# Kernel optimization log

Measured on AMD Instinct MI355X. Metric: run time of the kernel, lower is better.

## Reference

```python
import jax, jax.numpy as jnp
import numpy as np
import math

B, C, H, W = 8, 256, 64, 64
G = 32           # norm_groups
IMG_C = 3        # image_channels * wavelet_components
EPS = 1e-5


def group_norm(x, gamma, beta):
    # x: [B, C, H, W]; normalize over (C//G, H, W) within each of G groups
    b, c, h, w = x.shape
    xg = x.reshape(b, G, c // G, h, w)
    mean = xg.mean(axis=(2, 3, 4), keepdims=True)
    var = xg.var(axis=(2, 3, 4), keepdims=True)
    xg = (xg - mean) * jax.lax.rsqrt(var + EPS)
    x = xg.reshape(b, c, h, w)
    return x * gamma[None, :, None, None] + beta[None, :, None, None]


def conv1x1(x, weight):
    # weight: [out_c, in_c]; 1x1 conv == channel matmul
    return jnp.einsum('oc,bchw->bohw', weight, x)


def setup_inputs() -> dict:
    key = jax.random.key(0)
    ks = jax.random.split(key, 8)
    s_q = 1.0 / math.sqrt(IMG_C)
    s_kv = 1.0 / math.sqrt(C)
    return {
        'input': jax.random.normal(ks[0], (B, C, H, W), jnp.float32),
        'quary': jax.random.normal(ks[1], (B, IMG_C, H, W), jnp.float32),
        'gn_weight': jnp.ones((C,), jnp.float32),
        'gn_bias': jnp.zeros((C,), jnp.float32),
        'w_q': jax.random.uniform(ks[2], (C, IMG_C), jnp.float32, -s_q, s_q),
        'w_kv': jax.random.uniform(ks[3], (2 * C, C), jnp.float32, -s_kv, s_kv),
        'w_out': jax.random.uniform(ks[4], (C, C), jnp.float32, -s_kv, s_kv),
        'b_out': jax.random.uniform(ks[5], (C,), jnp.float32, -s_kv, s_kv),
    }


def reference(input, quary, gn_weight, gn_bias, w_q, w_kv, w_out, b_out):
    b, c, h, w = input.shape
    norm = group_norm(input, gn_weight, gn_bias)
    kv = conv1x1(norm, w_kv)                      # [B, 2C, H, W]
    key_t, value = kv[:, :c], kv[:, c:]           # each [B, C, H, W]
    q = conv1x1(quary, w_q)                       # [B, C, H, W]
    # attention over all spatial positions, single head, head_dim = C
    attn = jnp.einsum('bchw,bcyx->bhwyx', q, key_t) / math.sqrt(c)
    attn = jax.nn.softmax(attn.reshape(b, h, w, h * w), axis=-1)
    attn = attn.reshape(b, h, w, h, w)
    out = jnp.einsum('bhwyx,bcyx->bchw', attn, value)  # [B, C, H, W]
    out = conv1x1(out, w_out) + b_out[None, :, None, None]
    return out + input
```

## Files before the change

### kernel.cpp

```cpp
#include <hip/hip_runtime.h>

typedef unsigned short u16;
typedef unsigned int   u32;
typedef float  f32x4  __attribute__((ext_vector_type(4)));
typedef float  fltx4  __attribute__((ext_vector_type(4)));
typedef float  f32x2  __attribute__((ext_vector_type(2)));
typedef short  bf16x8 __attribute__((ext_vector_type(8)));
typedef u32    u32x4  __attribute__((ext_vector_type(4)));
typedef u32    u32x2  __attribute__((ext_vector_type(2)));

#define CDIM 256
#define NPIX 4096
#define QSCALE 0.09016843736f

__device__ __forceinline__ u16 f2bf(float f) {
  u32 u = __builtin_bit_cast(u32, f);
  u += 0x7fffu + ((u >> 16) & 1u);
  return (u16)(u >> 16);
}
__device__ __forceinline__ float bf2f(u16 h) {
  return __builtin_bit_cast(float, (u32)h << 16);
}

#if __has_builtin(__builtin_amdgcn_exp2f)
#define FEXP2 __builtin_amdgcn_exp2f
#else
#define FEXP2 exp2f
#endif

#define LO2(v) __builtin_shufflevector(v, v, 0, 1)
#define HI2(v) __builtin_shufflevector(v, v, 2, 3)

union U8 { bf16x8 v; u16 u[8]; u32 w[4]; };

__device__ __forceinline__ void llds16(u16* lds_base, const u16* gsrc) {
  __builtin_amdgcn_global_load_lds(
      (const __attribute__((address_space(1))) unsigned int*)gsrc,
      (__attribute__((address_space(3))) unsigned int*)lds_base, 16, 0, 0);
}

__global__ __launch_bounds__(256) void prep(const float* __restrict__ wkv,
                                            const float* __restrict__ wout,
                                            const float* __restrict__ wq,
                                            u16* __restrict__ w16,
                                            float* __restrict__ wq3p) {
  const int blk = blockIdx.x, tid = threadIdx.x;
  if (blk < 4) {
    const float* s = (blk < 2 ? wkv + 65536 : wout) + (blk & 1) * 32768;
    u16* d = w16 + (blk >> 1) * 65536 + (blk & 1) * 32768;
    for (int i = tid * 4; i < 32768; i += 1024) {
      fltx4 v = *(const fltx4*)(s + i);
      u32x2 o;
      o[0] = (u32)f2bf(v[0]) | ((u32)f2bf(v[1]) << 16);
      o[1] = (u32)f2bf(v[2]) | ((u32)f2bf(v[3]) << 16);
      *(u32x2*)(d + i) = o;
    }
  } else {
    const int p = blk - 4, c = tid;
    float a0 = 0.f, a1 = 0.f, a2 = 0.f;
    for (int o = p * 64; o < p * 64 + 64; ++o) {
      float kv = wkv[o * 256 + c];
      a0 += wq[o * 3 + 0] * kv;
      a1 += wq[o * 3 + 1] * kv;
      a2 += wq[o * 3 + 2] * kv;
    }
    float* dst = wq3p + (p * 256 + c) * 4;
    dst[0] = a0 * QSCALE; dst[1] = a1 * QSCALE; dst[2] = a2 * QSCALE; dst[3] = 0.f;
  }
}

__global__ __launch_bounds__(1024) void gn_stats(const float* __restrict__ x,
                                                 float* __restrict__ stats) {
  int bg = blockIdx.x;
  const float* base = x + (long)bg * 32768;
  float s = 0.f, s2 = 0.f;
  for (int i = threadIdx.x; i < 8192; i += 1024) {
    fltx4 v = ((const fltx4*)base)[i];
    s  += v[0] + v[1] + v[2] + v[3];
    s2 += v[0]*v[0] + v[1]*v[1] + v[2]*v[2] + v[3]*v[3];
  }
  for (int off = 1; off < 64; off <<= 1) {
    s  += __shfl_xor(s, off);
    s2 += __shfl_xor(s2, off);
  }
  __shared__ float red[32];
  int w = threadIdx.x >> 6;
  if ((threadIdx.x & 63) == 0) { red[w] = s; red[16 + w] = s2; }
  __syncthreads();
  if (threadIdx.x < 16) {
    s  = red[threadIdx.x];
    s2 = red[16 + threadIdx.x];
    for (int off = 1; off < 16; off <<= 1) {
      s  += __shfl_xor(s, off);
      s2 += __shfl_xor(s2, off);
    }
    if (threadIdx.x == 0) {
      float mean = s * (1.f / 32768.f);
      float var  = s2 * (1.f / 32768.f) - mean * mean;
      stats[bg * 2]     = mean;
      stats[bg * 2 + 1] = rsqrtf(var + 1e-5f);
    }
  }
}

__global__ __launch_bounds__(256) void gn_apply(const float* __restrict__ x,
                                                const float* __restrict__ stats,
                                                const float* __restrict__ gamma,
                                                const float* __restrict__ beta,
                                                const float* __restrict__ wq3p,
                                                u16* __restrict__ normT,
                                                float* __restrict__ K3x,
                                                float* __restrict__ K3y,
                                                float* __restrict__ K3z) {
  __shared__ u16 tile[256 * 66];
  __shared__ float wl4[256 * 4];
  __shared__ float part[4][64][4];
  const int tid = threadIdx.x;
  const int b = blockIdx.y, nb = blockIdx.x * 64;
  const int nIn = tid & 63, c4 = tid >> 6;
  {
    const f32x4* wp = (const f32x4*)wq3p;
    *(f32x4*)&wl4[tid * 4] = wp[tid] + wp[256 + tid] + wp[512 + tid] + wp[768 + tid];
  }
  const float* xb = x + (long)b * (CDIM * NPIX);
  #pragma unroll 4
  for (int p = 0; p < 64; ++p) {
    int c = c4 * 64 + p;
    int g = c >> 3;
    float mean = stats[(b * 32 + g) * 2];
    float rstd = stats[(b * 32 + g) * 2 + 1];
    float v = xb[(long)c * NPIX + nb + nIn];
    tile[c * 66 + nIn] = f2bf((v - mean) * rstd * gamma[c] + beta[c]);
  }
  __syncthreads();
  u16* nT = normT + ((long)b * NPIX + nb) * CDIM;
  #pragma unroll 8
  for (int nl = 0; nl < 64; ++nl)
    nT[(long)nl * CDIM + tid] = tile[tid * 66 + nl];
  {
    float a0 = 0.f, a1 = 0.f, a2 = 0.f;
    #pragma unroll 8
    for (int cc = 0; cc < 64; ++cc) {
      int c = c4 * 64 + cc;
      float v = bf2f(tile[c * 66 + nIn]);
      const f32x4 wv = *(const f32x4*)&wl4[c * 4];
      a0 += v * wv[0]; a1 += v * wv[1]; a2 += v * wv[2];
    }
    part[c4][nIn][0] = a0; part[c4][nIn][1] = a1; part[c4][nIn][2] = a2;
  }
  __syncthreads();
  if (c4 == 0) {
    float s0 = part[0][nIn][0] + part[1][nIn][0] + part[2][nIn][0] + part[3][nIn][0];
    float s1 = part[0][nIn][1] + part[1][nIn][1] + part[2][nIn][1] + part[3][nIn][1];
    float s2 = part[0][nIn][2] + part[1][nIn][2] + part[2][nIn][2] + part[3][nIn][2];
    long idx = (long)b * NPIX + nb + nIn;
    K3x[idx] = s0; K3y[idx] = s1; K3z[idx] = s2;
  }
}

template <bool FINAL, bool MERGE>
__global__ __launch_bounds__(256, 2) void gemm_nt(
    const void* __restrict__ Ap, const void* __restrict__ Bp,
    const void* __restrict__ Bp2, const float* __restrict__ ls,
    void* __restrict__ Dp,
    const float* __restrict__ bias, const float* __restrict__ resid,
    int M, int N, long aBS, long bBS, long dBS, long rBS) {
  __shared__ u16 Als[128 * 72];
  __shared__ u16 Bls[128 * 72];
  __shared__ float invB[128];
  const int tid = threadIdx.x;
  const int lane = tid & 63;
  const int m = lane & 15, quad = lane >> 4;
  const int wid = tid >> 6;
  const int wm = wid & 1, wn = wid >> 1;
  const int m0 = blockIdx.x * 128, n0 = blockIdx.y * 128;
  const int bz = blockIdx.z;

  if constexpr (MERGE) {
    if (tid < 128) {
      long n = (long)bz * 4096 + n0 + tid;
      invB[tid] = 1.f / (ls[n] + ls[32768 + n]);
    }
    __syncthreads();
  }

  f32x4 acc[4][4] = {};

  for (int ks = 0; ks < 4; ++ks) {
    const int kb = ks * 64;
    if (ks) __syncthreads();
    {
      const u16* src = (const u16*)Ap + aBS * bz;
      #pragma unroll
      for (int it = 0; it < 4; ++it) {
        int idx = it * 2048 + tid * 8;
        int r = idx >> 6, c = idx & 63;
        *(u32x4*)&Als[r * 72 + c] = *(const u32x4*)(src + (long)(m0 + r) * CDIM + kb + c);
      }
    }
    if constexpr (MERGE) {
      const u16* s0 = (const u16*)Bp  + bBS * bz;
      const u16* s1 = (const u16*)Bp2 + bBS * bz;
      #pragma unroll
      for (int it = 0; it < 4; ++it) {
        int idx = it * 2048 + tid * 8;
        int r = idx >> 6, c = idx & 63;
        long off = (long)(n0 + r) * CDIM + kb + c;
        u32x4 A  = *(const u32x4*)(s0 + off);
        u32x4 Bq = *(const u32x4*)(s1 + off);
        float inv = invB[r];
        u32x4 o;
        #pragma unroll
        for (int i = 0; i < 4; ++i) {
          float lo = (bf2f((u16)(A[i] & 0xffff)) + bf2f((u16)(Bq[i] & 0xffff))) * inv;
          float hi = (bf2f((u16)(A[i] >> 16))    + bf2f((u16)(Bq[i] >> 16)))    * inv;
          o[i] = (u32)f2bf(lo) | ((u32)f2bf(hi) << 16);
        }
        *(u32x4*)&Bls[r * 72 + c] = o;
      }
    } else {
      const u16* src = (const u16*)Bp + bBS * bz;
      #pragma unroll
      for (int it = 0; it < 4; ++it) {
        int idx = it * 2048 + tid * 8;
        int r = idx >> 6, c = idx & 63;
        *(u32x4*)&Bls[r * 72 + c] = *(const u32x4*)(src + (long)(n0 + r) * CDIM + kb + c);
      }
    }
    __syncthreads();
    #pragma unroll
    for (int s = 0; s < 2; ++s) {
      bf16x8 av[4], bv[4];
      #pragma unroll
      for (int i = 0; i < 4; ++i)
        av[i] = *(const bf16x8*)&Als[(wm * 64 + i * 16 + m) * 72 + s * 32 + quad * 8];
      #pragma unroll
      for (int i = 0; i < 4; ++i)
        bv[i] = *(const bf16x8*)&Bls[(wn * 64 + i * 16 + m) * 72 + s * 32 + quad * 8];
      #pragma unroll
      for (int mi = 0; mi < 4; ++mi)
        #pragma unroll
        for (int ni = 0; ni < 4; ++ni)
          acc[mi][ni] = __builtin_amdgcn_mfma_f32_16x16x32_bf16(av[mi], bv[ni], acc[mi][ni], 0, 0, 0);
    }
  }

  const int row0 = m0 + wm * 64;
  const int col0 = n0 + wn * 64 + m;
  if constexpr (FINAL) {
    float* out = (float*)Dp + dBS * bz;
    const float* res = resid + rBS * bz;
    #pragma unroll
    for (int mi = 0; mi < 4; ++mi)
      #pragma unroll
      for (int r = 0; r < 4; ++r) {
        int row = row0 + mi * 16 + quad * 4 + r;
        float bs = bias[row];
        #pragma unroll
        for (int ni = 0; ni < 4; ++ni) {
          long off = (long)row * N + col0 + ni * 16;
          out[off] = acc[mi][ni][r] + bs + res[off];
        }
      }
  } else {
    u16* out = (u16*)Dp + dBS * bz;
    #pragma unroll
    for (int mi = 0; mi < 4; ++mi)
      #pragma unroll
      for (int r = 0; r < 4; ++r) {
        int row = row0 + mi * 16 + quad * 4 + r;
        #pragma unroll
        for (int ni = 0; ni < 4; ++ni)
          out[(long)row * N + col0 + ni * 16] = f2bf(acc[mi][ni][r]);
      }
  }
}

#define MFMA16(a, bfr, c) __builtin_amdgcn_mfma_f32_16x16x32_bf16(a, bfr, c, 0, 0, 0)

#define P_LOAD(ks, JB)                                                      \
  {                                                                         \
    const int jo_ = (JB) + (ks) * 32 + quad * 8;                            \
    kx0 = *(const fltx4*)(Kx + jo_); kx1 = *(const fltx4*)(Kx + jo_ + 4);   \
    ky0 = *(const fltx4*)(Ky + jo_); ky1 = *(const fltx4*)(Ky + jo_ + 4);   \
    kz0 = *(const fltx4*)(Kz + jo_); kz1 = *(const fltx4*)(Kz + jo_ + 4);   \
  }

#define P_EXP(PB, ks)                                                       \
  {                                                                         \
    f32x2 xc_[4] = {LO2(kx0), HI2(kx0), LO2(kx1), HI2(kx1)};                \
    f32x2 yc_[4] = {LO2(ky0), HI2(ky0), LO2(ky1), HI2(ky1)};                \
    f32x2 zc_[4] = {LO2(kz0), HI2(kz0), LO2(kz1), HI2(kz1)};                \
    _Pragma("unroll")                                                       \
    for (int qm_ = 0; qm_ < 2; ++qm_) {                                     \
      _Pragma("unroll")                                                     \
      for (int c2_ = 0; c2_ < 4; ++c2_) {                                   \
        f32x2 s_ = xc_[c2_] * y2[qm_][0] + yc_[c2_] * y2[qm_][1]            \
                 + zc_[c2_] * y2[qm_][2];                                   \
        float p0_ = FEXP2(s_[0]);                                           \
        float p1_ = FEXP2(s_[1]);                                           \
        u32 r0_ = __builtin_bit_cast(u32, p0_) + 0x8000u;                   \
        u32 r1_ = __builtin_bit_cast(u32, p1_) + 0x8000u;                   \
        PB[qm_][ks].w[c2_] = (r0_ >> 16) | (r1_ & 0xffff0000u);             \
        f32x2 pv_; pv_[0] = p0_; pv_[1] = p1_;                              \
        lsv[qm_] += pv_;                                                    \
      }                                                                     \
    }                                                                       \
  }

#define PV_GROUP(PB, CT0)                                                   \
  _Pragma("unroll")                                                         \
  for (int ct_ = (CT0); ct_ < (CT0) + 4; ++ct_) {                           \
    int c_ = ct_ * 16 + m;                                                  \
    bf16x8 a0_ = *(const bf16x8*)&Vb[c_ * 64 + (((quad)     ^ (c_ & 7)) << 3)]; \
    bf16x8 a1_ = *(const bf16x8*)&Vb[c_ * 64 + (((4 + quad) ^ (c_ & 7)) << 3)]; \
    acc[0][ct_] = MFMA16(a0_, PB[0][0].v, acc[0][ct_]);                     \
    acc[1][ct_] = MFMA16(a0_, PB[1][0].v, acc[1][ct_]);                     \
    acc[0][ct_] = MFMA16(a1_, PB[0][1].v, acc[0][ct_]);                     \
    acc[1][ct_] = MFMA16(a1_, PB[1][1].v, acc[1][ct_]);                     \
  }

__global__ __launch_bounds__(256, 2) void attn_kernel(
    const float* __restrict__ quary,
    const float* __restrict__ K3x, const float* __restrict__ K3y,
    const float* __restrict__ K3z,
    const u16* __restrict__ V, u16* __restrict__ Op0, u16* __restrict__ Op1,
    float* __restrict__ lsum) {
  __shared__ u16 VLS[2][256 * 64];
  const int lane = threadIdx.x & 63, w = threadIdx.x >> 6;
  const int m = lane & 15, quad = lane >> 4;
  const int b = blockIdx.z, half = blockIdx.y;
  const int qb = blockIdx.x * 128 + w * 32;

  f32x2 y2[2][3];
  #pragma unroll
  for (int qm = 0; qm < 2; ++qm) {
    int n = qb + qm * 16 + m;
    float q0 = quary[b * 12288 + n];
    float q1 = quary[b * 12288 + 4096 + n];
    float q2 = quary[b * 12288 + 8192 + n];
    y2[qm][0][0] = q0; y2[qm][0][1] = q0;
    y2[qm][1][0] = q1; y2[qm][1][1] = q1;
    y2[qm][2][0] = q2; y2[qm][2][1] = q2;
  }

  const float* Kx = K3x + (long)b * NPIX + half * 2048;
  const float* Ky = K3y + (long)b * NPIX + half * 2048;
  const float* Kz = K3z + (long)b * NPIX + half * 2048;
  const u16* VG = V + (long)b * CDIM * NPIX + half * 2048;

  int srcV[8];
  #pragma unroll
  for (int i = 0; i < 8; ++i) {
    int c = (w * 8 + i) * 8 + (lane >> 3);
    srcV[i] = c * NPIX + (((lane & 7) ^ (c & 7)) << 3);
  }

  f32x2 lsv[2] = {};
  f32x4 acc[2][16] = {};
  U8 pbA[2][2], pbB[2][2];
  fltx4 kx0, kx1, ky0, ky1, kz0, kz1;

  #pragma unroll
  for (int i = 0; i < 8; ++i)
    llds16(VLS[0] + (w * 8 + i) * 512, VG + srcV[i]);

  P_LOAD(0, 0); P_EXP(pbA, 0);
  P_LOAD(1, 0); P_EXP(pbA, 1);

  for (int kt = 0; kt < 31; ++kt) {
    __syncthreads();
    #pragma unroll
    for (int i = 0; i < 8; ++i)
      llds16(VLS[(kt + 1) & 1] + (w * 8 + i) * 512, VG + srcV[i] + (kt + 1) * 64);
    const u16* Vb = VLS[kt & 1];
    const int JB = (kt + 1) * 64;

    P_LOAD(0, JB);
    PV_GROUP(pbA, 0);
    PV_GROUP(pbA, 4);
    P_EXP(pbB, 0);
    P_LOAD(1, JB);
    PV_GROUP(pbA, 8);
    PV_GROUP(pbA, 12);
    P_EXP(pbB, 1);

    pbA[0][0] = pbB[0][0]; pbA[0][1] = pbB[0][1];
    pbA[1][0] = pbB[1][0]; pbA[1][1] = pbB[1][1];
  }
  {
    __syncthreads();
    const u16* Vb = VLS[1];
    PV_GROUP(pbA, 0);
    PV_GROUP(pbA, 4);
    PV_GROUP(pbA, 8);
    PV_GROUP(pbA, 12);
  }

  u16* OpB = (half ? Op1 : Op0);
  #pragma unroll
  for (int qm = 0; qm < 2; ++qm) {
    int n = qb + qm * 16 + m;
    u16* row = OpB + ((long)b * NPIX + n) * CDIM + quad * 4;
    #pragma unroll
    for (int ct = 0; ct < 16; ++ct) {
      u32x2 o;
      o[0] = (u32)f2bf(acc[qm][ct][0]) | ((u32)f2bf(acc[qm][ct][1]) << 16);
      o[1] = (u32)f2bf(acc[qm][ct][2]) | ((u32)f2bf(acc[qm][ct][3]) << 16);
      *(u32x2*)(row + ct * 16) = o;
    }
    float ls = lsv[qm][0] + lsv[qm][1];
    ls += __shfl_xor(ls, 16);
    ls += __shfl_xor(ls, 32);
    if (lane < 16)
      lsum[(long)half * 32768 + (long)b * NPIX + n] = ls;
  }
}

extern "C" void kernel_launch(void* const* d_in, const int* in_sizes, int n_in,
                              void* d_out, int out_size, void* d_ws, size_t ws_size,
                              hipStream_t stream) {
  (void)in_sizes; (void)n_in; (void)out_size; (void)ws_size;
  const float* input = (const float*)d_in[0];
  const float* quary = (const float*)d_in[1];
  const float* gnw   = (const float*)d_in[2];
  const float* gnb   = (const float*)d_in[3];
  const float* wq    = (const float*)d_in[4];
  const float* wkv   = (const float*)d_in[5];
  const float* wout  = (const float*)d_in[6];
  const float* bout  = (const float*)d_in[7];
  float* out = (float*)d_out;

  char* ws = (char*)d_ws;
  float* stats = (float*)ws;
  float* wq3p  = (float*)(ws + 4096);
  float* lsum  = (float*)(ws + 20480);
  float* K3x   = (float*)(ws + 282624);
  float* K3y   = (float*)(ws + 413696);
  float* K3z   = (float*)(ws + 544768);
  u16* w16   = (u16*)(ws + 675840);
  u16* normT = (u16*)(ws + 937984);
  u16* Vv    = (u16*)(ws + 937984 + 1L * 16777216);
  u16* Op0   = normT;
  u16* Op1   = (u16*)(ws + 937984 + 2L * 16777216);

  const long S = (long)NPIX * CDIM;

  prep<<<8, 256, 0, stream>>>(wkv, wout, wq, w16, wq3p);
  gn_stats<<<256, 1024, 0, stream>>>(input, stats);
  gn_apply<<<dim3(64, 8), 256, 0, stream>>>(input, stats, gnw, gnb, wq3p,
                                            normT, K3x, K3y, K3z);
  gemm_nt<false, false><<<dim3(2, 32, 8), 256, 0, stream>>>(
      w16, normT, nullptr, nullptr, Vv, nullptr, nullptr, 256, 4096, 0, S, S, 0);
  attn_kernel<<<dim3(32, 2, 8), 256, 0, stream>>>(quary, K3x, K3y, K3z, Vv, Op0, Op1, lsum);
  gemm_nt<true, true><<<dim3(2, 32, 8), 256, 0, stream>>>(
      w16 + 65536, Op0, Op1, lsum, out, bout, input, 256, 4096, 0, S, S, S);
}
```

Before: 240.5 us.

## Split attention work across 8 waves with 16 query rows each

The attention kernel now launches 512 threads per block, and each of the 8 waves handles 16 query rows instead of 32. This halves the per-thread accumulator and P-fragment register footprint, which allows higher occupancy (launch bounds 512,4). The exp computation is split into finer half-steps interleaved with the PV MFMA groups. In exchange, each V tile loaded into LDS is reused by each wave across fewer queries per MFMA operand load, which doubles the LDS read traffic per unit of compute.

```diff
diff --git a/kernel.cpp b/kernel.cpp
--- a/kernel.cpp
+++ b/kernel.cpp
@@ -278,49 +278,47 @@
 
 #define MFMA16(a, bfr, c) __builtin_amdgcn_mfma_f32_16x16x32_bf16(a, bfr, c, 0, 0, 0)
 
-#define P_LOAD(ks, JB)                                                      \
+#define PH_LOAD(ks, h)                                                      \
   {                                                                         \
-    const int jo_ = (JB) + (ks) * 32 + quad * 8;                            \
-    kx0 = *(const fltx4*)(Kx + jo_); kx1 = *(const fltx4*)(Kx + jo_ + 4);   \
-    ky0 = *(const fltx4*)(Ky + jo_); ky1 = *(const fltx4*)(Ky + jo_ + 4);   \
-    kz0 = *(const fltx4*)(Kz + jo_); kz1 = *(const fltx4*)(Kz + jo_ + 4);   \
-  }
-
-#define P_EXP(PB, ks)                                                       \
+    const int jo_ = JB + (ks) * 32 + quad * 8 + (h) * 4;                    \
+    kxa = *(const fltx4*)(Kx + jo_);                                        \
+    kya = *(const fltx4*)(Ky + jo_);                                        \
+    kza = *(const fltx4*)(Kz + jo_);                                        \
+  }
+
+#define PH_EXP(PB, ks, h)                                                   \
   {                                                                         \
-    f32x2 xc_[4] = {LO2(kx0), HI2(kx0), LO2(kx1), HI2(kx1)};                \
-    f32x2 yc_[4] = {LO2(ky0), HI2(ky0), LO2(ky1), HI2(ky1)};                \
-    f32x2 zc_[4] = {LO2(kz0), HI2(kz0), LO2(kz1), HI2(kz1)};                \
-    _Pragma("unroll")                                                       \
-    for (int qm_ = 0; qm_ < 2; ++qm_) {                                     \
-      _Pragma("unroll")                                                     \
-      for (int c2_ = 0; c2_ < 4; ++c2_) {                                   \
-        f32x2 s_ = xc_[c2_] * y2[qm_][0] + yc_[c2_] * y2[qm_][1]            \
-                 + zc_[c2_] * y2[qm_][2];                                   \
-        float p0_ = FEXP2(s_[0]);                                           \
-        float p1_ = FEXP2(s_[1]);                                           \
-        u32 r0_ = __builtin_bit_cast(u32, p0_) + 0x8000u;                   \
-        u32 r1_ = __builtin_bit_cast(u32, p1_) + 0x8000u;                   \
-        PB[qm_][ks].w[c2_] = (r0_ >> 16) | (r1_ & 0xffff0000u);             \
-        f32x2 pv_; pv_[0] = p0_; pv_[1] = p1_;                              \
-        lsv[qm_] += pv_;                                                    \
-      }                                                                     \
-    }                                                                       \
-  }
-
-#define PV_GROUP(PB, CT0)                                                   \
+    f32x2 xc0_ = LO2(kxa), xc1_ = HI2(kxa);                                 \
+    f32x2 yc0_ = LO2(kya), yc1_ = HI2(kya);                                 \
+    f32x2 zc0_ = LO2(kza), zc1_ = HI2(kza);                                 \
+    f32x2 s0_ = xc0_ * y2[0] + yc0_ * y2[1] + zc0_ * y2[2];                 \
+    f32x2 s1_ = xc1_ * y2[0] + yc1_ * y2[1] + zc1_ * y2[2];                 \
+    float p0_ = FEXP2(s0_[0]);                                              \
+    float p1_ = FEXP2(s0_[1]);                                              \
+    float p2_ = FEXP2(s1_[0]);                                              \
+    float p3_ = FEXP2(s1_[1]);                                              \
+    u32 r0_ = __builtin_bit_cast(u32, p0_) + 0x8000u;                       \
+    u32 r1_ = __builtin_bit_cast(u32, p1_) + 0x8000u;                       \
+    u32 r2_ = __builtin_bit_cast(u32, p2_) + 0x8000u;                       \
+    u32 r3_ = __builtin_bit_cast(u32, p3_) + 0x8000u;                       \
+    PB[ks].w[(h) * 2]     = (r0_ >> 16) | (r1_ & 0xffff0000u);              \
+    PB[ks].w[(h) * 2 + 1] = (r2_ >> 16) | (r3_ & 0xffff0000u);              \
+    f32x2 pa_; pa_[0] = p0_; pa_[1] = p1_;                                  \
+    f32x2 pb_; pb_[0] = p2_; pb_[1] = p3_;                                  \
+    lsv += pa_ + pb_;                                                       \
+  }
+
+#define PV_G(PB, CT0)                                                       \
   _Pragma("unroll")                                                         \
   for (int ct_ = (CT0); ct_ < (CT0) + 4; ++ct_) {                           \
     int c_ = ct_ * 16 + m;                                                  \
     bf16x8 a0_ = *(const bf16x8*)&Vb[c_ * 64 + (((quad)     ^ (c_ & 7)) << 3)]; \
     bf16x8 a1_ = *(const bf16x8*)&Vb[c_ * 64 + (((4 + quad) ^ (c_ & 7)) << 3)]; \
-    acc[0][ct_] = MFMA16(a0_, PB[0][0].v, acc[0][ct_]);                     \
-    acc[1][ct_] = MFMA16(a0_, PB[1][0].v, acc[1][ct_]);                     \
-    acc[0][ct_] = MFMA16(a1_, PB[0][1].v, acc[0][ct_]);                     \
-    acc[1][ct_] = MFMA16(a1_, PB[1][1].v, acc[1][ct_]);                     \
-  }
-
-__global__ __launch_bounds__(256, 2) void attn_kernel(
+    acc[ct_] = MFMA16(a0_, PB[0].v, acc[ct_]);                              \
+    acc[ct_] = MFMA16(a1_, PB[1].v, acc[ct_]);                              \
+  }
+
+__global__ __launch_bounds__(512, 4) void attn_kernel(
     const float* __restrict__ quary,
     const float* __restrict__ K3x, const float* __restrict__ K3y,
     const float* __restrict__ K3z,
@@ -330,18 +328,17 @@
   const int lane = threadIdx.x & 63, w = threadIdx.x >> 6;
   const int m = lane & 15, quad = lane >> 4;
   const int b = blockIdx.z, half = blockIdx.y;
-  const int qb = blockIdx.x * 128 + w * 32;
-
-  f32x2 y2[2][3];
-  #pragma unroll
-  for (int qm = 0; qm < 2; ++qm) {
-    int n = qb + qm * 16 + m;
+  const int qb = blockIdx.x * 128 + w * 16;
+
+  f32x2 y2[3];
+  {
+    int n = qb + m;
     float q0 = quary[b * 12288 + n];
     float q1 = quary[b * 12288 + 4096 + n];
     float q2 = quary[b * 12288 + 8192 + n];
-    y2[qm][0][0] = q0; y2[qm][0][1] = q0;
-    y2[qm][1][0] = q1; y2[qm][1][1] = q1;
-    y2[qm][2][0] = q2; y2[qm][2][1] = q2;
+    y2[0][0] = q0; y2[0][1] = q0;
+    y2[1][0] = q1; y2[1][1] = q1;
+    y2[2][0] = q2; y2[2][1] = q2;
   }
 
   const float* Kx = K3x + (long)b * NPIX + half * 2048;
@@ -349,67 +346,74 @@
   const float* Kz = K3z + (long)b * NPIX + half * 2048;
   const u16* VG = V + (long)b * CDIM * NPIX + half * 2048;
 
-  int srcV[8];
+  int srcV[4];
   #pragma unroll
-  for (int i = 0; i < 8; ++i) {
-    int c = (w * 8 + i) * 8 + (lane >> 3);
+  for (int i = 0; i < 4; ++i) {
+    int c = (w * 4 + i) * 8 + (lane >> 3);
     srcV[i] = c * NPIX + (((lane & 7) ^ (c & 7)) << 3);
   }
 
-  f32x2 lsv[2] = {};
-  f32x4 acc[2][16] = {};
-  U8 pbA[2][2], pbB[2][2];
-  fltx4 kx0, kx1, ky0, ky1, kz0, kz1;
+  f32x2 lsv = {};
+  f32x4 acc[16] = {};
+  U8 pbA[2], pbB[2];
+  fltx4 kxa, kya, kza;
 
   #pragma unroll
-  for (int i = 0; i < 8; ++i)
-    llds16(VLS[0] + (w * 8 + i) * 512, VG + srcV[i]);
-
-  P_LOAD(0, 0); P_EXP(pbA, 0);
-  P_LOAD(1, 0); P_EXP(pbA, 1);
+  for (int i = 0; i < 4; ++i)
+    llds16(VLS[0] + (w * 4 + i) * 512, VG + srcV[i]);
+
+  {
+    const int JB = 0;
+    PH_LOAD(0, 0); PH_EXP(pbA, 0, 0);
+    PH_LOAD(0, 1); PH_EXP(pbA, 0, 1);
+    PH_LOAD(1, 0); PH_EXP(pbA, 1, 0);
+    PH_LOAD(1, 1); PH_EXP(pbA, 1, 1);
+  }
 
   for (int kt = 0; kt < 31; ++kt) {
     __syncthreads();
     #pragma unroll
-    for (int i = 0; i < 8; ++i)
-      llds16(VLS[(kt + 1) & 1] + (w * 8 + i) * 512, VG + srcV[i] + (kt + 1) * 64);
+    for (int i = 0; i < 4; ++i)
+      llds16(VLS[(kt + 1) & 1] + (w * 4 + i) * 512, VG + srcV[i] + (kt + 1) * 64);
     const u16* Vb = VLS[kt & 1];
     const int JB = (kt + 1) * 64;
 
-    P_LOAD(0, JB);
-    PV_GROUP(pbA, 0);
-    PV_GROUP(pbA, 4);
-    P_EXP(pbB, 0);
-    P_LOAD(1, JB);
-    PV_GROUP(pbA, 8);
-    PV_GROUP(pbA, 12);
-    P_EXP(pbB, 1);
-
-    pbA[0][0] = pbB[0][0]; pbA[0][1] = pbB[0][1];
-    pbA[1][0] = pbB[1][0]; pbA[1][1] = pbB[1][1];
+    PH_LOAD(0, 0);
+    PV_G(pbA, 0);
+    PH_EXP(pbB, 0, 0);
+    PH_LOAD(0, 1);
+    PV_G(pbA, 4);
+    PH_EXP(pbB, 0, 1);
+    PH_LOAD(1, 0);
+    PV_G(pbA, 8);
+    PH_EXP(pbB, 1, 0);
+    PH_LOAD(1, 1);
+    PV_G(pbA, 12);
+    PH_EXP(pbB, 1, 1);
+
+    pbA[0] = pbB[0]; pbA[1] = pbB[1];
   }
   {
     __syncthreads();
     const u16* Vb = VLS[1];
-    PV_GROUP(pbA, 0);
-    PV_GROUP(pbA, 4);
-    PV_GROUP(pbA, 8);
-    PV_GROUP(pbA, 12);
+    PV_G(pbA, 0);
+    PV_G(pbA, 4);
+    PV_G(pbA, 8);
+    PV_G(pbA, 12);
   }
 
   u16* OpB = (half ? Op1 : Op0);
-  #pragma unroll
-  for (int qm = 0; qm < 2; ++qm) {
-    int n = qb + qm * 16 + m;
+  {
+    int n = qb + m;
     u16* row = OpB + ((long)b * NPIX + n) * CDIM + quad * 4;
     #pragma unroll
     for (int ct = 0; ct < 16; ++ct) {
       u32x2 o;
-      o[0] = (u32)f2bf(acc[qm][ct][0]) | ((u32)f2bf(acc[qm][ct][1]) << 16);
-      o[1] = (u32)f2bf(acc[qm][ct][2]) | ((u32)f2bf(acc[qm][ct][3]) << 16);
+      o[0] = (u32)f2bf(acc[ct][0]) | ((u32)f2bf(acc[ct][1]) << 16);
+      o[1] = (u32)f2bf(acc[ct][2]) | ((u32)f2bf(acc[ct][3]) << 16);
       *(u32x2*)(row + ct * 16) = o;
     }
-    float ls = lsv[qm][0] + lsv[qm][1];
+    float ls = lsv[0] + lsv[1];
     ls += __shfl_xor(ls, 16);
     ls += __shfl_xor(ls, 32);
     if (lane < 16)
@@ -452,7 +456,7 @@
                                             normT, K3x, K3y, K3z);
   gemm_nt<false, false><<<dim3(2, 32, 8), 256, 0, stream>>>(
       w16, normT, nullptr, nullptr, Vv, nullptr, nullptr, 256, 4096, 0, S, S, 0);
-  attn_kernel<<<dim3(32, 2, 8), 256, 0, stream>>>(quary, K3x, K3y, K3z, Vv, Op0, Op1, lsum);
+  attn_kernel<<<dim3(32, 2, 8), 512, 0, stream>>>(quary, K3x, K3y, K3z, Vv, Op0, Op1, lsum);
   gemm_nt<true, true><<<dim3(2, 32, 8), 256, 0, stream>>>(
       w16 + 65536, Op0, Op1, lsum, out, bout, input, 256, 4096, 0, S, S, S);
 }
```

After: 261.2 us. 1.09x slower.

## Fuse value projection GEMM into group-norm apply kernel, dropping normT buffer

Applied to the files above, without the earlier changes.

The group-norm apply kernel now keeps the normalized tile in LDS in pixel-major layout and directly runs the V projection with bf16 MFMAs, writing V to global memory. This removes the separate V GEMM launch and the round trip of the normalized activations through global memory. Each block reads the full 256x256 weight matrix from global or L2 memory without LDS staging, and the V stores are scattered 2-byte writes. The GEMM template parameter is also renamed, with no change in behavior.

```diff
diff --git a/kernel.cpp b/kernel.cpp
--- a/kernel.cpp
+++ b/kernel.cpp
@@ -103,48 +103,57 @@
   }
 }
 
-__global__ __launch_bounds__(256) void gn_apply(const float* __restrict__ x,
+#define TSTR 264
+__global__ __launch_bounds__(256) void gn_fused(const float* __restrict__ x,
                                                 const float* __restrict__ stats,
                                                 const float* __restrict__ gamma,
                                                 const float* __restrict__ beta,
                                                 const float* __restrict__ wq3p,
-                                                u16* __restrict__ normT,
+                                                const u16* __restrict__ w16v,
+                                                u16* __restrict__ Vv,
                                                 float* __restrict__ K3x,
                                                 float* __restrict__ K3y,
                                                 float* __restrict__ K3z) {
-  __shared__ u16 tile[256 * 66];
+  __shared__ u16 tile[64 * TSTR];
   __shared__ float wl4[256 * 4];
   __shared__ float part[4][64][4];
   const int tid = threadIdx.x;
   const int b = blockIdx.y, nb = blockIdx.x * 64;
   const int nIn = tid & 63, c4 = tid >> 6;
+  const int lane = tid & 63;
+  const int m = lane & 15, quad = lane >> 4;
   {
     const f32x4* wp = (const f32x4*)wq3p;
     *(f32x4*)&wl4[tid * 4] = wp[tid] + wp[256 + tid] + wp[512 + tid] + wp[768 + tid];
   }
   const float* xb = x + (long)b * (CDIM * NPIX);
-  #pragma unroll 4
-  for (int p = 0; p < 64; ++p) {
-    int c = c4 * 64 + p;
-    int g = c >> 3;
-    float mean = stats[(b * 32 + g) * 2];
-    float rstd = stats[(b * 32 + g) * 2 + 1];
-    float v = xb[(long)c * NPIX + nb + nIn];
-    tile[c * 66 + nIn] = f2bf((v - mean) * rstd * gamma[c] + beta[c]);
+  #pragma unroll
+  for (int p8 = 0; p8 < 8; ++p8) {
+    U8 pk;
+    #pragma unroll
+    for (int e = 0; e < 8; ++e) {
+      int c = c4 * 64 + p8 * 8 + e;
+      int g = c >> 3;
+      float mean = stats[(b * 32 + g) * 2];
+      float rstd = stats[(b * 32 + g) * 2 + 1];
+      float v = xb[(long)c * NPIX + nb + nIn];
+      pk.u[e] = f2bf((v - mean) * rstd * gamma[c] + beta[c]);
+    }
+    *(bf16x8*)&tile[nIn * TSTR + c4 * 64 + p8 * 8] = pk.v;
   }
   __syncthreads();
-  u16* nT = normT + ((long)b * NPIX + nb) * CDIM;
-  #pragma unroll 8
-  for (int nl = 0; nl < 64; ++nl)
-    nT[(long)nl * CDIM + tid] = tile[tid * 66 + nl];
   {
     float a0 = 0.f, a1 = 0.f, a2 = 0.f;
-    #pragma unroll 8
-    for (int cc = 0; cc < 64; ++cc) {
-      int c = c4 * 64 + cc;
-      float v = bf2f(tile[c * 66 + nIn]);
-      const f32x4 wv = *(const f32x4*)&wl4[c * 4];
-      a0 += v * wv[0]; a1 += v * wv[1]; a2 += v * wv[2];
+    #pragma unroll
+    for (int p8 = 0; p8 < 8; ++p8) {
+      U8 v; v.v = *(const bf16x8*)&tile[nIn * TSTR + c4 * 64 + p8 * 8];
+      #pragma unroll
+      for (int e = 0; e < 8; ++e) {
+        int c = c4 * 64 + p8 * 8 + e;
+        float f = bf2f(v.u[e]);
+        const f32x4 wv = *(const f32x4*)&wl4[c * 4];
+        a0 += f * wv[0]; a1 += f * wv[1]; a2 += f * wv[2];
+      }
     }
     part[c4][nIn][0] = a0; part[c4][nIn][1] = a1; part[c4][nIn][2] = a2;
   }
@@ -156,12 +165,40 @@
     long idx = (long)b * NPIX + nb + nIn;
     K3x[idx] = s0; K3y[idx] = s1; K3z[idx] = s2;
   }
-}
-
-template <bool FINAL, bool MERGE>
+  f32x4 acc[4][4] = {};
+  #pragma unroll
+  for (int ks = 0; ks < 8; ++ks) {
+    const int kb = ks * 32;
+    bf16x8 av[4], bv[4];
+    #pragma unroll
+    for (int i = 0; i < 4; ++i)
+      av[i] = *(const bf16x8*)&w16v[(c4 * 64 + i * 16 + m) * 256 + kb + quad * 8];
+    #pragma unroll
+    for (int i = 0; i < 4; ++i)
+      bv[i] = *(const bf16x8*)&tile[(i * 16 + m) * TSTR + kb + quad * 8];
+    #pragma unroll
+    for (int mi = 0; mi < 4; ++mi)
+      #pragma unroll
+      for (int ni = 0; ni < 4; ++ni)
+        acc[mi][ni] = __builtin_amdgcn_mfma_f32_16x16x32_bf16(av[mi], bv[ni], acc[mi][ni], 0, 0, 0);
+  }
+  u16* Vb = Vv + (long)b * (CDIM * NPIX);
+  #pragma unroll
+  for (int mi = 0; mi < 4; ++mi)
+    #pragma unroll
+    for (int r = 0; r < 4; ++r) {
+      int o = c4 * 64 + mi * 16 + quad * 4 + r;
+      #pragma unroll
+      for (int ni = 0; ni < 4; ++ni)
+        Vb[(long)o * NPIX + nb + ni * 16 + m] = f2bf(acc[mi][ni][r]);
+    }
+}
+
+template <bool FINAL, int WAYS>
 __global__ __launch_bounds__(256, 2) void gemm_nt(
-    const void* __restrict__ Ap, const void* __restrict__ Bp,
-    const void* __restrict__ Bp2, const float* __restrict__ ls,
+    const void* __restrict__ Ap,
+    const void* __restrict__ B0, const void* __restrict__ B1,
+    const float* __restrict__ ls,
     void* __restrict__ Dp,
     const float* __restrict__ bias, const float* __restrict__ resid,
     int M, int N, long aBS, long bBS, long dBS, long rBS) {
@@ -176,7 +213,7 @@
   const int m0 = blockIdx.x * 128, n0 = blockIdx.y * 128;
   const int bz = blockIdx.z;
 
-  if constexpr (MERGE) {
+  if constexpr (WAYS > 0) {
     if (tid < 128) {
       long n = (long)bz * 4096 + n0 + tid;
       invB[tid] = 1.f / (ls[n] + ls[32768 + n]);
@@ -198,28 +235,28 @@
         *(u32x4*)&Als[r * 72 + c] = *(const u32x4*)(src + (long)(m0 + r) * CDIM + kb + c);
       }
     }
-    if constexpr (MERGE) {
-      const u16* s0 = (const u16*)Bp  + bBS * bz;
-      const u16* s1 = (const u16*)Bp2 + bBS * bz;
+    if constexpr (WAYS > 0) {
+      const u16* s0 = (const u16*)B0 + bBS * bz;
+      const u16* s1 = (const u16*)B1 + bBS * bz;
       #pragma unroll
       for (int it = 0; it < 4; ++it) {
         int idx = it * 2048 + tid * 8;
         int r = idx >> 6, c = idx & 63;
         long off = (long)(n0 + r) * CDIM + kb + c;
-        u32x4 A  = *(const u32x4*)(s0 + off);
-        u32x4 Bq = *(const u32x4*)(s1 + off);
+        u32x4 A0 = *(const u32x4*)(s0 + off);
+        u32x4 A1 = *(const u32x4*)(s1 + off);
         float inv = invB[r];
         u32x4 o;
         #pragma unroll
         for (int i = 0; i < 4; ++i) {
-          float lo = (bf2f((u16)(A[i] & 0xffff)) + bf2f((u16)(Bq[i] & 0xffff))) * inv;
-          float hi = (bf2f((u16)(A[i] >> 16))    + bf2f((u16)(Bq[i] >> 16)))    * inv;
+          float lo = (bf2f((u16)(A0[i] & 0xffff)) + bf2f((u16)(A1[i] & 0xffff))) * inv;
+          float hi = (bf2f((u16)(A0[i] >> 16))    + bf2f((u16)(A1[i] >> 16)))    * inv;
           o[i] = (u32)f2bf(lo) | ((u32)f2bf(hi) << 16);
         }
         *(u32x4*)&Bls[r * 72 + c] = o;
       }
     } else {
-      const u16* src = (const u16*)Bp + bBS * bz;
+      const u16* src = (const u16*)B0 + bBS * bz;
       #pragma unroll
       for (int it = 0; it < 4; ++it) {
         int idx = it * 2048 + tid * 8;
@@ -439,20 +476,18 @@
   float* K3y   = (float*)(ws + 413696);
   float* K3z   = (float*)(ws + 544768);
   u16* w16   = (u16*)(ws + 675840);
-  u16* normT = (u16*)(ws + 937984);
-  u16* Vv    = (u16*)(ws + 937984 + 1L * 16777216);
-  u16* Op0   = normT;
-  u16* Op1   = (u16*)(ws + 937984 + 2L * 16777216);
+  const long base = 937984;
+  u16* Vv    = (u16*)(ws + base);
+  u16* Op0   = (u16*)(ws + base + 1L * 16777216);
+  u16* Op1   = (u16*)(ws + base + 2L * 16777216);
 
   const long S = (long)NPIX * CDIM;
 
   prep<<<8, 256, 0, stream>>>(wkv, wout, wq, w16, wq3p);
   gn_stats<<<256, 1024, 0, stream>>>(input, stats);
-  gn_apply<<<dim3(64, 8), 256, 0, stream>>>(input, stats, gnw, gnb, wq3p,
-                                            normT, K3x, K3y, K3z);
-  gemm_nt<false, false><<<dim3(2, 32, 8), 256, 0, stream>>>(
-      w16, normT, nullptr, nullptr, Vv, nullptr, nullptr, 256, 4096, 0, S, S, 0);
+  gn_fused<<<dim3(64, 8), 256, 0, stream>>>(input, stats, gnw, gnb, wq3p,
+                                            w16, Vv, K3x, K3y, K3z);
   attn_kernel<<<dim3(32, 2, 8), 256, 0, stream>>>(quary, K3x, K3y, K3z, Vv, Op0, Op1, lsum);
-  gemm_nt<true, true><<<dim3(2, 32, 8), 256, 0, stream>>>(
+  gemm_nt<true, 2><<<dim3(2, 32, 8), 256, 0, stream>>>(
       w16 + 65536, Op0, Op1, lsum, out, bout, input, 256, 4096, 0, S, S, S);
 }
```

Result: faster. 233.1 us (-3.1%).
